# Kernel optimization log

Measured on AMD Instinct MI355X. Metric: run time of the kernel, lower is better.

## Reference

```python
import jax, jax.numpy as jnp
import numpy as np

B, T, S, D = 32, 1024, 1024, 512
VOCAB = 1000
INSERT_TOK = jnp.array([1, 2], dtype=jnp.int64)


def setup_inputs() -> dict:
    key = jax.random.key(0)
    k1, k2, k3, k4, k5 = jax.random.split(key, 5)
    input_var = jax.random.randint(k1, (B, T), 0, VOCAB, dtype=jnp.int64)
    output = jax.random.normal(k2, (B, T, D), jnp.float32)
    context = jax.random.normal(k3, (B, S, D), jnp.float32)
    # nn.Linear(2*dim, dim): weight [D, 2D], bias [D]
    W = jax.random.normal(k4, (D, 2 * D), jnp.float32) / np.sqrt(2 * D)
    b = jax.random.normal(k5, (D,), jnp.float32) * 0.01
    return {"input_var": input_var, "output": output, "context": context,
            "di": 0, "W": W, "b": b}


def _hard_align(input_var, src_len):
    """Replicates the python double-loop: sequential 'inserted' counter per batch.
    Returns (j, valid): j[b,i] = column of the 1.0 in attn row i (torch negative
    indices wrapped), valid[b,i] = whether row i gets any 1.0 at all."""
    bsz, tgt_len = input_var.shape
    flags = jnp.isin(input_var, INSERT_TOK)  # [B,T] is token an insert token

    def step(inserted, xi):
        i, flag = xi  # i: scalar position, flag: [B]
        cond = (src_len >= i - inserted)                    # gate, per batch
        ins2 = inserted + jnp.where(cond & flag, 1, 0)      # increment before write
        j = i - ins2 - 1
        j = jnp.where(j < 0, j + src_len, j)                # torch negative-index wrap
        return ins2, (j, cond)

    idxs = jnp.arange(1, tgt_len, dtype=jnp.int32)
    init = jnp.zeros((bsz,), jnp.int32)  # init_inserted()
    _, (j_rows, valid) = jax.lax.scan(step, init, (idxs, flags[:, 1:].T))
    j_rows = j_rows.T      # [B,T-1]
    valid = valid.T        # [B,T-1]
    # row 0: attn[b,0,0] = 1.0 always
    j_full = jnp.concatenate([jnp.zeros((bsz, 1), j_rows.dtype), j_rows], axis=1)
    valid_full = jnp.concatenate([jnp.ones((bsz, 1), bool), valid], axis=1)
    return j_full, valid_full


def reference(input_var, output, context, di, W, b):
    bsz, tgt_len, hid = output.shape
    src_len = context.shape[1]
    j, valid = _hard_align(input_var, src_len)              # [B,T], [B,T]
    vf = valid[:, :, None].astype(output.dtype)
    # hard one-hot attention matrix (as the module materializes it)
    attn = jax.nn.one_hot(j, src_len, dtype=output.dtype) * vf  # [B,T,S]
    # mix = bmm(attn, context) == masked gather of context rows
    mix = jnp.take_along_axis(context, j[:, :, None].astype(jnp.int32), axis=1) * vf
    combined = jnp.concatenate([mix, output], axis=-1)      # [B,T,2D]
    out = jnp.tanh(combined @ W.T + b)                      # [B,T,D]
    return out, attn
```

## Files before the change

### kernel.cpp

```cpp
#include <hip/hip_runtime.h>
#include <hip/hip_bf16.h>

#define B_ 32
#define T_ 1024
#define S_ 1024
#define D_ 512
#define M_ (B_*T_)
#define N_ D_
#define K_ (2*D_)

typedef __attribute__((ext_vector_type(8))) short bf16x8;
typedef __attribute__((ext_vector_type(4))) float f32x4;

__device__ inline unsigned short f2bf(float x) {
    union { float f; unsigned u; } v; v.f = x;
    unsigned r = v.u + 0x7FFFu + ((v.u >> 16) & 1u);
    return (unsigned short)(r >> 16);
}

__global__ void align_kernel(const int* __restrict__ iv, int* __restrict__ jbuf) {
    const int b = blockIdx.x;
    const int lane = threadIdx.x;
    const int* row = iv + b * T_;
    int f[16];
    int local = 0;
    const int t0 = lane * 16;
    #pragma unroll
    for (int q = 0; q < 16; ++q) {
        const int t = t0 + q;
        const int tok = row[t];
        const int fl = (t > 0 && (tok == 1 || tok == 2)) ? 1 : 0;
        f[q] = fl;
        local += fl;
    }
    int incl = local;
    #pragma unroll
    for (int off = 1; off < 64; off <<= 1) {
        const int up = __shfl_up(incl, off, 64);
        if (lane >= off) incl += up;
    }
    int run = incl - local;
    #pragma unroll
    for (int q = 0; q < 16; ++q) {
        const int t = t0 + q;
        run += f[q];
        int j;
        if (t == 0) {
            j = 0;
        } else {
            j = t - run - 1;
            if (j < 0) j += S_;
        }
        jbuf[b * T_ + t] = j;
    }
}

__global__ __launch_bounds__(256)
void attn_fill(const int* __restrict__ jbuf, float* __restrict__ attn) {
    const int row = blockIdx.x;
    const int j = jbuf[row];
    const int c4 = threadIdx.x;
    f32x4 v = {0.f, 0.f, 0.f, 0.f};
    if ((j >> 2) == c4) v[j & 3] = 1.0f;
    ((f32x4*)(attn + (size_t)row * S_))[c4] = v;
}

__global__ void pack_w(const float* __restrict__ W, unsigned short* __restrict__ Wbf) {
    const int idx = blockIdx.x * blockDim.x + threadIdx.x;
    const f32x4 a = ((const f32x4*)W)[idx * 2];
    const f32x4 c = ((const f32x4*)W)[idx * 2 + 1];
    union { bf16x8 v; unsigned short u[8]; } pk;
    pk.u[0] = f2bf(a[0]); pk.u[1] = f2bf(a[1]); pk.u[2] = f2bf(a[2]); pk.u[3] = f2bf(a[3]);
    pk.u[4] = f2bf(c[0]); pk.u[5] = f2bf(c[1]); pk.u[6] = f2bf(c[2]); pk.u[7] = f2bf(c[3]);
    *(bf16x8*)(Wbf + (size_t)idx * 8) = pk.v;
}

__global__ void pack_a(const float* __restrict__ ctx, const float* __restrict__ outp,
                       const int* __restrict__ jbuf, unsigned short* __restrict__ Abf) {
    const int idx = blockIdx.x * blockDim.x + threadIdx.x;
    const int m  = idx >> 7;
    const int k0 = (idx & 127) * 8;
    const float* src;
    if (k0 < D_) {
        const int b = m >> 10;
        src = ctx + ((size_t)(b * S_ + jbuf[m])) * D_ + k0;
    } else {
        src = outp + (size_t)m * D_ + (k0 - D_);
    }
    const f32x4 a = ((const f32x4*)src)[0];
    const f32x4 c = ((const f32x4*)src)[1];
    union { bf16x8 v; unsigned short u[8]; } pk;
    pk.u[0] = f2bf(a[0]); pk.u[1] = f2bf(a[1]); pk.u[2] = f2bf(a[2]); pk.u[3] = f2bf(a[3]);
    pk.u[4] = f2bf(c[0]); pk.u[5] = f2bf(c[1]); pk.u[6] = f2bf(c[2]); pk.u[7] = f2bf(c[3]);
    *(bf16x8*)(Abf + (size_t)m * K_ + k0) = pk.v;
}

#define BM 128
#define BN 128
#define BK 64

template <bool PACKED>
__global__ __launch_bounds__(256)
void gemm_bt_tanh(const unsigned short* __restrict__ Abf,
                  const unsigned short* __restrict__ Wbf,
                  const float* __restrict__ bias,
                  float* __restrict__ out,
                  const float* __restrict__ ctx,
                  const float* __restrict__ outp,
                  const int* __restrict__ jbuf) {
    __shared__ unsigned short As[BM * BK];
    __shared__ unsigned short Bs[BN * BK];

    const int tid  = threadIdx.x;
    const int lane = tid & 63;
    const int wave = tid >> 6;
    const int wm = wave >> 1, wn = wave & 1;
    const int l16 = lane & 15, quad = lane >> 4;

    const int bm = blockIdx.x & 255;
    const int bn = blockIdx.x >> 8;
    const int mBase = bm * BM;
    const int nBase = bn * BN;

    f32x4 acc[4][4] = {};

    for (int ko = 0; ko < K_; ko += BK) {
        #pragma unroll
        for (int it = 0; it < 4; ++it) {
            const int chunk = it * 256 + tid;
            const int row = chunk >> 3;
            const int k8  = (chunk & 7) * 8;
            if (PACKED) {
                const unsigned short* gA = Abf + (size_t)(mBase + row) * K_ + ko + k8;
                __builtin_amdgcn_global_load_lds(
                    (const __attribute__((address_space(1))) void*)gA,
                    (__attribute__((address_space(3))) void*)(As + chunk * 8), 16, 0, 0);
            } else {
                const int kg = ko + k8;
                const int m = mBase + row;
                const float* src;
                if (kg < D_) {
                    const int b = m >> 10;
                    src = ctx + ((size_t)(b * S_ + jbuf[m])) * D_ + kg;
                } else {
                    src = outp + (size_t)m * D_ + (kg - D_);
                }
                const f32x4 a = ((const f32x4*)src)[0];
                const f32x4 c = ((const f32x4*)src)[1];
                union { bf16x8 v; unsigned short u[8]; } pk;
                pk.u[0]=f2bf(a[0]); pk.u[1]=f2bf(a[1]); pk.u[2]=f2bf(a[2]); pk.u[3]=f2bf(a[3]);
                pk.u[4]=f2bf(c[0]); pk.u[5]=f2bf(c[1]); pk.u[6]=f2bf(c[2]); pk.u[7]=f2bf(c[3]);
                *(bf16x8*)(As + chunk * 8) = pk.v;
            }
        }
        #pragma unroll
        for (int it = 0; it < 4; ++it) {
            const int chunk = it * 256 + tid;
            const int row = chunk >> 3;
            const int k8  = (chunk & 7) * 8;
            const unsigned short* gB = Wbf + (size_t)(nBase + row) * K_ + ko + k8;
            __builtin_amdgcn_global_load_lds(
                (const __attribute__((address_space(1))) void*)gB,
                (__attribute__((address_space(3))) void*)(Bs + chunk * 8), 16, 0, 0);
        }
        __syncthreads();

        #pragma unroll
        for (int ks = 0; ks < 2; ++ks) {
            bf16x8 af[4], bfr[4];
            #pragma unroll
            for (int mt = 0; mt < 4; ++mt)
                af[mt] = *(const bf16x8*)&As[(wm * 64 + mt * 16 + l16) * BK + ks * 32 + quad * 8];
            #pragma unroll
            for (int nt = 0; nt < 4; ++nt)
                bfr[nt] = *(const bf16x8*)&Bs[(wn * 64 + nt * 16 + l16) * BK + ks * 32 + quad * 8];
            #pragma unroll
            for (int mt = 0; mt < 4; ++mt)
                #pragma unroll
                for (int nt = 0; nt < 4; ++nt)
                    acc[mt][nt] = __builtin_amdgcn_mfma_f32_16x16x32_bf16(
                        af[mt], bfr[nt], acc[mt][nt], 0, 0, 0);
        }
        __syncthreads();
    }

    #pragma unroll
    for (int nt = 0; nt < 4; ++nt) {
        const int n = nBase + wn * 64 + nt * 16 + l16;
        const float bv = bias[n];
        #pragma unroll
        for (int mt = 0; mt < 4; ++mt) {
            #pragma unroll
            for (int r = 0; r < 4; ++r) {
                const int m = mBase + wm * 64 + mt * 16 + quad * 4 + r;
                out[(size_t)m * N_ + n] = tanhf(acc[mt][nt][r] + bv);
            }
        }
    }
}

extern "C" void kernel_launch(void* const* d_in, const int* in_sizes, int n_in,
                              void* d_out, int out_size, void* d_ws, size_t ws_size,
                              hipStream_t stream) {
    const int*   iv   = (const int*)d_in[0];
    const float* outp = (const float*)d_in[1];
    const float* ctx  = (const float*)d_in[2];
    const float* W    = (const float*)d_in[4];
    const float* bias = (const float*)d_in[5];

    float* out  = (float*)d_out;
    float* attn = out + (size_t)M_ * N_;

    int* jbuf = (int*)d_ws;
    unsigned short* Wbf = (unsigned short*)((char*)d_ws + (size_t)M_ * 4);
    unsigned short* Abf = (unsigned short*)((char*)d_ws + (size_t)M_ * 4 + (size_t)N_ * K_ * 2);
    const size_t need_full = (size_t)M_ * 4 + (size_t)N_ * K_ * 2 + (size_t)M_ * K_ * 2;

    align_kernel<<<B_, 64, 0, stream>>>(iv, jbuf);
    attn_fill<<<M_, 256, 0, stream>>>(jbuf, attn);
    pack_w<<<(N_ * K_ / 8) / 256, 256, 0, stream>>>(W, Wbf);

    if (ws_size >= need_full) {
        pack_a<<<(M_ * K_ / 8) / 256, 256, 0, stream>>>(ctx, outp, jbuf, Abf);
        gemm_bt_tanh<true><<<(M_ / BM) * (N_ / BN), 256, 0, stream>>>(
            Abf, Wbf, bias, out, ctx, outp, jbuf);
    } else {
        gemm_bt_tanh<false><<<(M_ / BM) * (N_ / BN), 256, 0, stream>>>(
            Abf, Wbf, bias, out, ctx, outp, jbuf);
    }
}
```

Measured before the change: 381.2 us.

## Fuse attn fill into A packing, swizzle LDS tiles, use fast tanh

Merges the one-hot attention fill into the A-packing kernel so that one launch writes both the bf16 A rows and the attn rows. It adds an XOR swizzle to the LDS layout of the A and B tiles in the GEMM to avoid bank conflicts on the fragment reads. It replaces tanhf in the epilogue with an exp2/rcp approximation. The fallback path now also writes Abf, which can overflow a small workspace, and the fast tanh loses some accuracy.

```diff
diff --git a/kernel.cpp b/kernel.cpp
--- a/kernel.cpp
+++ b/kernel.cpp
@@ -16,6 +16,16 @@
     union { float f; unsigned u; } v; v.f = x;
     unsigned r = v.u + 0x7FFFu + ((v.u >> 16) & 1u);
     return (unsigned short)(r >> 16);
+}
+
+__device__ inline float fast_tanh(float x) {
+#if __has_builtin(__builtin_amdgcn_exp2f) && __has_builtin(__builtin_amdgcn_rcpf)
+    const float e = __builtin_amdgcn_exp2f(x * 2.885390082f);
+    const float r = __builtin_amdgcn_rcpf(e + 1.0f);
+    return 1.0f - 2.0f * r;
+#else
+    return tanhf(x);
+#endif
 }
 
 __global__ void align_kernel(const int* __restrict__ iv, int* __restrict__ jbuf) {
@@ -55,16 +65,6 @@
     }
 }
 
-__global__ __launch_bounds__(256)
-void attn_fill(const int* __restrict__ jbuf, float* __restrict__ attn) {
-    const int row = blockIdx.x;
-    const int j = jbuf[row];
-    const int c4 = threadIdx.x;
-    f32x4 v = {0.f, 0.f, 0.f, 0.f};
-    if ((j >> 2) == c4) v[j & 3] = 1.0f;
-    ((f32x4*)(attn + (size_t)row * S_))[c4] = v;
-}
-
 __global__ void pack_w(const float* __restrict__ W, unsigned short* __restrict__ Wbf) {
     const int idx = blockIdx.x * blockDim.x + threadIdx.x;
     const f32x4 a = ((const f32x4*)W)[idx * 2];
@@ -75,15 +75,24 @@
     *(bf16x8*)(Wbf + (size_t)idx * 8) = pk.v;
 }
 
-__global__ void pack_a(const float* __restrict__ ctx, const float* __restrict__ outp,
-                       const int* __restrict__ jbuf, unsigned short* __restrict__ Abf) {
-    const int idx = blockIdx.x * blockDim.x + threadIdx.x;
-    const int m  = idx >> 7;
-    const int k0 = (idx & 127) * 8;
+__global__ __launch_bounds__(256)
+void pack_a_attn(const float* __restrict__ ctx, const float* __restrict__ outp,
+                 const int* __restrict__ jbuf, unsigned short* __restrict__ Abf,
+                 float* __restrict__ attn) {
+    const int m0 = blockIdx.x * 2;
+    const int tid = threadIdx.x;
+    const int r  = tid >> 7;
+    const int kc = tid & 127;
+    const int m  = m0 + r;
+    const int k0 = kc * 8;
+    const int j0 = jbuf[m0];
+    const int j1 = jbuf[m0 + 1];
+
+    const int jm = r ? j1 : j0;
     const float* src;
     if (k0 < D_) {
         const int b = m >> 10;
-        src = ctx + ((size_t)(b * S_ + jbuf[m])) * D_ + k0;
+        src = ctx + ((size_t)(b * S_ + jm)) * D_ + k0;
     } else {
         src = outp + (size_t)m * D_ + (k0 - D_);
     }
@@ -93,6 +102,13 @@
     pk.u[0] = f2bf(a[0]); pk.u[1] = f2bf(a[1]); pk.u[2] = f2bf(a[2]); pk.u[3] = f2bf(a[3]);
     pk.u[4] = f2bf(c[0]); pk.u[5] = f2bf(c[1]); pk.u[6] = f2bf(c[2]); pk.u[7] = f2bf(c[3]);
     *(bf16x8*)(Abf + (size_t)m * K_ + k0) = pk.v;
+
+    f32x4 v0 = {0.f, 0.f, 0.f, 0.f};
+    f32x4 v1 = {0.f, 0.f, 0.f, 0.f};
+    if ((j0 >> 2) == tid) v0[j0 & 3] = 1.0f;
+    if ((j1 >> 2) == tid) v1[j1 & 3] = 1.0f;
+    ((f32x4*)(attn + (size_t)m0 * S_))[tid] = v0;
+    ((f32x4*)(attn + (size_t)(m0 + 1) * S_))[tid] = v1;
 }
 
 #define BM 128
@@ -129,14 +145,15 @@
         for (int it = 0; it < 4; ++it) {
             const int chunk = it * 256 + tid;
             const int row = chunk >> 3;
-            const int k8  = (chunk & 7) * 8;
+            const int kc  = chunk & 7;
+            const int gk8 = (kc ^ (row & 7)) * 8;
             if (PACKED) {
-                const unsigned short* gA = Abf + (size_t)(mBase + row) * K_ + ko + k8;
+                const unsigned short* gA = Abf + (size_t)(mBase + row) * K_ + ko + gk8;
                 __builtin_amdgcn_global_load_lds(
                     (const __attribute__((address_space(1))) void*)gA,
                     (__attribute__((address_space(3))) void*)(As + chunk * 8), 16, 0, 0);
             } else {
-                const int kg = ko + k8;
+                const int kg = ko + gk8;
                 const int m = mBase + row;
                 const float* src;
                 if (kg < D_) {
@@ -157,8 +174,9 @@
         for (int it = 0; it < 4; ++it) {
             const int chunk = it * 256 + tid;
             const int row = chunk >> 3;
-            const int k8  = (chunk & 7) * 8;
-            const unsigned short* gB = Wbf + (size_t)(nBase + row) * K_ + ko + k8;
+            const int kc  = chunk & 7;
+            const int gk8 = (kc ^ (row & 7)) * 8;
+            const unsigned short* gB = Wbf + (size_t)(nBase + row) * K_ + ko + gk8;
             __builtin_amdgcn_global_load_lds(
                 (const __attribute__((address_space(1))) void*)gB,
                 (__attribute__((address_space(3))) void*)(Bs + chunk * 8), 16, 0, 0);
@@ -169,11 +187,17 @@
         for (int ks = 0; ks < 2; ++ks) {
             bf16x8 af[4], bfr[4];
             #pragma unroll
-            for (int mt = 0; mt < 4; ++mt)
-                af[mt] = *(const bf16x8*)&As[(wm * 64 + mt * 16 + l16) * BK + ks * 32 + quad * 8];
-            #pragma unroll
-            for (int nt = 0; nt < 4; ++nt)
-                bfr[nt] = *(const bf16x8*)&Bs[(wn * 64 + nt * 16 + l16) * BK + ks * 32 + quad * 8];
+            for (int mt = 0; mt < 4; ++mt) {
+                const int r = wm * 64 + mt * 16 + l16;
+                const int q = ks * 4 + quad;
+                af[mt] = *(const bf16x8*)&As[(r * 8 + (q ^ (r & 7))) * 8];
+            }
+            #pragma unroll
+            for (int nt = 0; nt < 4; ++nt) {
+                const int r = wn * 64 + nt * 16 + l16;
+                const int q = ks * 4 + quad;
+                bfr[nt] = *(const bf16x8*)&Bs[(r * 8 + (q ^ (r & 7))) * 8];
+            }
             #pragma unroll
             for (int mt = 0; mt < 4; ++mt)
                 #pragma unroll
@@ -193,7 +217,7 @@
             #pragma unroll
             for (int r = 0; r < 4; ++r) {
                 const int m = mBase + wm * 64 + mt * 16 + quad * 4 + r;
-                out[(size_t)m * N_ + n] = tanhf(acc[mt][nt][r] + bv);
+                out[(size_t)m * N_ + n] = fast_tanh(acc[mt][nt][r] + bv);
             }
         }
     }
@@ -217,14 +241,14 @@
     const size_t need_full = (size_t)M_ * 4 + (size_t)N_ * K_ * 2 + (size_t)M_ * K_ * 2;
 
     align_kernel<<<B_, 64, 0, stream>>>(iv, jbuf);
-    attn_fill<<<M_, 256, 0, stream>>>(jbuf, attn);
     pack_w<<<(N_ * K_ / 8) / 256, 256, 0, stream>>>(W, Wbf);
 
     if (ws_size >= need_full) {
-        pack_a<<<(M_ * K_ / 8) / 256, 256, 0, stream>>>(ctx, outp, jbuf, Abf);
+        pack_a_attn<<<M_ / 2, 256, 0, stream>>>(ctx, outp, jbuf, Abf, attn);
         gemm_bt_tanh<true><<<(M_ / BM) * (N_ / BN), 256, 0, stream>>>(
             Abf, Wbf, bias, out, ctx, outp, jbuf);
     } else {
+        pack_a_attn<<<M_ / 2, 256, 0, stream>>>(ctx, outp, jbuf, Abf, attn);
         gemm_bt_tanh<false><<<(M_ / BM) * (N_ / BN), 256, 0, stream>>>(
             Abf, Wbf, bias, out, ctx, outp, jbuf);
     }
```

Result: no change. 379.8 us (-0.4%).
